# Kernel tuning notes

Measured on AMD Instinct MI355X. Metric: run time of the kernel, lower is better.

Reference implementation:

```python
import jax, jax.numpy as jnp
import numpy as np

T, H, I, E, K = 2048, 1024, 768, 32, 4  # tokens, hidden, expert intermediate, n_experts, top_k


def setup_inputs() -> dict:
    key = jax.random.key(0)
    k0, k1, k2, k3, k4 = jax.random.split(key, 5)
    scale = 0.02
    return {
        "x": jax.random.normal(k0, (T, H), dtype=jnp.float32),
        "gate_w": jax.random.normal(k1, (E, H), dtype=jnp.float32) * scale,   # router linear [E, H]
        "w_gate": jax.random.normal(k2, (E, I, H), dtype=jnp.float32) * scale,  # gate_proj per expert
        "w_up": jax.random.normal(k3, (E, I, H), dtype=jnp.float32) * scale,    # up_proj per expert
        "w_down": jax.random.normal(k4, (E, H, I), dtype=jnp.float32) * scale,  # down_proj per expert
    }


def reference(x, gate_w, w_gate, w_up, w_down):
    # Router: dense gate linear + softmax + top-k + renormalize
    logits = x @ gate_w.T                              # [T, E]
    probs = jax.nn.softmax(logits, axis=-1)
    top_w, top_i = jax.lax.top_k(probs, K)             # [T, K]
    top_w = top_w / jnp.sum(top_w, axis=-1, keepdims=True)  # renormalize=True
    # Dense combine weights [T, E] (zero for unselected experts)
    tok = jnp.arange(T, dtype=jnp.int32)[:, None]
    combine = jnp.zeros((T, E), dtype=x.dtype).at[tok, top_i].add(top_w)

    # Scan over experts: each expert is a SwiGLU MLP; masked-dense combine.
    def step(acc, ws):
        w1, w3, w2, ce = ws                            # [I,H], [I,H], [H,I], [T]
        h = (jax.nn.silu(x @ w1.T) * (x @ w3.T)) @ w2.T  # [T, H]
        return acc + ce[:, None] * h, None

    out, _ = jax.lax.scan(step, jnp.zeros_like(x), (w_gate, w_up, w_down, combine.T))
    return out
```

## Files before the change

### kernel.cpp

```cpp
#include <hip/hip_runtime.h>
#include <hip/hip_bf16.h>
#include <stdint.h>

#define T_TOK 2048
#define HDIM  1024
#define IDIM  768
#define NEXP  32
#define TOPK  4
#define NPAIR (T_TOK*TOPK)
#define MTILE 256
#define MAXMT 64

typedef __attribute__((ext_vector_type(8))) short bf16x8;
typedef __attribute__((ext_vector_type(4))) float f32x4;

__device__ __forceinline__ unsigned short f2bf(float f){
  union { float f; unsigned u; } v; v.f = f;
  unsigned r = (v.u + 0x7fffu + ((v.u >> 16) & 1u)) >> 16;
  return (unsigned short)r;
}

__global__ __launch_bounds__(256) void k_convert_x(const float* __restrict__ x,
                                                   ushort* __restrict__ xb){
  int idx = blockIdx.x*256 + threadIdx.x;
  float4 v = ((const float4*)x)[idx];
  ushort4 o; o.x=f2bf(v.x); o.y=f2bf(v.y); o.z=f2bf(v.z); o.w=f2bf(v.w);
  ((ushort4*)xb)[idx] = o;
}

__global__ __launch_bounds__(256) void k_router(const float* __restrict__ x,
                                                const float* __restrict__ gw,
                                                int* __restrict__ ei, float* __restrict__ wv,
                                                int* __restrict__ counts){
  int wid  = threadIdx.x >> 6;
  int lane = threadIdx.x & 63;
  int t = blockIdx.x*4 + wid;
  float xv[16];
  #pragma unroll
  for (int i=0;i<16;i++) xv[i] = x[t*HDIM + i*64 + lane];
  float p[NEXP];
  #pragma unroll
  for (int e=0;e<NEXP;e++){
    const float* w = gw + e*HDIM;
    float a = 0.f;
    #pragma unroll
    for (int i=0;i<16;i++) a = fmaf(xv[i], w[i*64+lane], a);
    #pragma unroll
    for (int off=32; off>=1; off>>=1) a += __shfl_xor(a, off, 64);
    p[e] = a;
  }
  float m = p[0];
  #pragma unroll
  for (int e=1;e<NEXP;e++) m = fmaxf(m, p[e]);
  #pragma unroll
  for (int e=0;e<NEXP;e++) p[e] = __expf(p[e]-m);
  unsigned used = 0; int sel[TOPK]; float sw[TOPK]; float wsum = 0.f;
  #pragma unroll
  for (int k=0;k<TOPK;k++){
    float best = -1.f; int bi = 0;
    #pragma unroll
    for (int e=0;e<NEXP;e++){
      bool ok = (((used>>e)&1u)==0u) && (p[e] > best);
      best = ok ? p[e] : best; bi = ok ? e : bi;
    }
    used |= 1u<<bi; sel[k]=bi; sw[k]=best; wsum += best;
  }
  if (lane==0){
    float inv = 1.f/wsum;
    #pragma unroll
    for (int k=0;k<TOPK;k++){
      ei[t*TOPK+k] = sel[k];
      wv[t*TOPK+k] = sw[k]*inv;
      atomicAdd(&counts[sel[k]], 1);
    }
  }
}

__global__ void k_offsets(const int* __restrict__ counts, int* __restrict__ offsets,
                          int* __restrict__ mtE, int* __restrict__ mtM0,
                          int* __restrict__ nmt){
  if (threadIdx.x==0 && blockIdx.x==0){
    int s=0;
    for (int e=0;e<NEXP;e++){ offsets[e]=s; s+=counts[e]; }
    offsets[NEXP]=s;
    int nm=0;
    for (int e=0;e<NEXP;e++){
      int ne = counts[e];
      for (int m0=0; m0<ne && nm<MAXMT; m0+=MTILE){ mtE[nm]=e; mtM0[nm]=m0; nm++; }
    }
    nmt[0]=nm;
  }
}

__global__ __launch_bounds__(256) void k_scatter(const int* __restrict__ ei,
                                                 const int* __restrict__ offsets,
                                                 int* __restrict__ cursor,
                                                 int* __restrict__ slot_tk,
                                                 int* __restrict__ tk_slot){
  int g = blockIdx.x*256 + threadIdx.x;
  int e = ei[g];
  int pos = atomicAdd(&cursor[e], 1);
  int slot = offsets[e] + pos;
  slot_tk[slot] = g;
  tk_slot[g] = slot;
}

__global__ __launch_bounds__(512,4) void k_gateup(const ushort* __restrict__ xb,
    const float* __restrict__ w1, const float* __restrict__ w3,
    const int* __restrict__ offsets, const int* __restrict__ slot_tk,
    const int* __restrict__ mtE, const int* __restrict__ mtM0, const int* __restrict__ nmt,
    ushort* __restrict__ act){
  int bi  = blockIdx.x;
  int mti = bi / 24;
  int it  = bi - mti*24;
  if (mti >= nmt[0]) return;
  int e    = mtE[mti];
  int m0   = mtM0[mti];
  int off0 = offsets[e];
  int ne   = offsets[e+1]-off0;
  int ibase = it*32;

  __shared__ int toks[256];
  __shared__ ushort Bls[2][2][32][68];

  int tid = threadIdx.x, wid = tid>>6, lane = tid&63;
  if (tid < 256){
    int slot = off0 + m0 + tid;
    int fb = slot_tk[off0] >> 2;
    toks[tid] = (m0 + tid < ne) ? (slot_tk[slot] >> 2) : fb;
  }
  int b_r = tid>>4, b_c4 = tid&15;
  const size_t wbase = (size_t)e * IDIM * HDIM;
  const float* bsrc0 = w1 + wbase + (size_t)(ibase+b_r)*HDIM + b_c4*4;
  const float* bsrc1 = w3 + wbase + (size_t)(ibase+b_r)*HDIM + b_c4*4;
  __syncthreads();

  const ushort* arow0 = xb + (size_t)toks[wid*32      + (lane&15)]*HDIM + (lane>>4)*8;
  const ushort* arow1 = xb + (size_t)toks[wid*32 + 16 + (lane&15)]*HDIM + (lane>>4)*8;

  f32x4 accg[2][2], accu[2][2];
  #pragma unroll
  for (int a=0;a<2;a++)
    #pragma unroll
    for (int b=0;b<2;b++){ accg[a][b]=(f32x4){0,0,0,0}; accu[a][b]=(f32x4){0,0,0,0}; }

  float4 bP[2], bQ[2];
  bf16x8 afA[4], afB[4];

  auto loadB = [&](int kb, float4* d){
    d[0] = *(const float4*)(bsrc0 + kb*64);
    d[1] = *(const float4*)(bsrc1 + kb*64);
  };
  auto loadA = [&](int kb, bf16x8* d){
    #pragma unroll
    for (int kk=0;kk<2;kk++){
      d[kk*2+0] = *(const bf16x8*)(arow0 + kb*64 + kk*32);
      d[kk*2+1] = *(const bf16x8*)(arow1 + kb*64 + kk*32);
    }
  };
  auto writeB = [&](int buf, const float4* s){
    #pragma unroll
    for (int m=0;m<2;m++){
      ushort4 o; o.x=f2bf(s[m].x); o.y=f2bf(s[m].y); o.z=f2bf(s[m].z); o.w=f2bf(s[m].w);
      *(ushort4*)(&Bls[buf][m][b_r][b_c4*4]) = o;
    }
  };
  auto compute = [&](int buf, const bf16x8* af){
    #pragma unroll
    for (int kk=0;kk<2;kk++){
      #pragma unroll
      for (int n=0;n<2;n++){
        bf16x8 bg = *(const bf16x8*)(&Bls[buf][0][n*16 + (lane&15)][kk*32 + (lane>>4)*8]);
        bf16x8 bu = *(const bf16x8*)(&Bls[buf][1][n*16 + (lane&15)][kk*32 + (lane>>4)*8]);
        #pragma unroll
        for (int m=0;m<2;m++){
          accg[m][n] = __builtin_amdgcn_mfma_f32_16x16x32_bf16(af[kk*2+m], bg, accg[m][n], 0,0,0);
          accu[m][n] = __builtin_amdgcn_mfma_f32_16x16x32_bf16(af[kk*2+m], bu, accu[m][n], 0,0,0);
        }
      }
    }
  };

  loadB(0, bP);
  loadA(0, afA);
  loadB(1, bQ);
  writeB(0, bP);
  __syncthreads();
  loadA(1, afB);

  for (int kb=0; kb<16; kb+=2){
    if (kb+2 < 16) loadB(kb+2, bP);
    compute(0, afA);
    if (kb+2 < 16) loadA(kb+2, afA);
    writeB(1, bQ);
    __syncthreads();
    if (kb+3 < 16) loadB(kb+3, bQ);
    compute(1, afB);
    if (kb+3 < 16) loadA(kb+3, afB);
    if (kb+2 < 16) writeB(0, bP);
    __syncthreads();
  }

  int nval = ne - m0; if (nval > 256) nval = 256;
  #pragma unroll
  for (int m=0;m<2;m++)
    #pragma unroll
    for (int n=0;n<2;n++)
      #pragma unroll
      for (int r=0;r<4;r++){
        int row = wid*32 + m*16 + (lane>>4)*4 + r;
        if (row < nval){
          float g = accg[m][n][r], u = accu[m][n][r];
          float sval = g / (1.f + __expf(-g)) * u;
          act[(size_t)(off0+m0+row)*IDIM + ibase + n*16 + (lane&15)] = f2bf(sval);
        }
      }
}

__global__ __launch_bounds__(512,4) void k_down(const ushort* __restrict__ act,
    const float* __restrict__ w2, const int* __restrict__ offsets,
    const int* __restrict__ mtE, const int* __restrict__ mtM0, const int* __restrict__ nmt,
    float* __restrict__ pout){
  int bi  = blockIdx.x;
  int mti = bi >> 4;
  int ht  = bi & 15;
  if (mti >= nmt[0]) return;
  int e    = mtE[mti];
  int m0   = mtM0[mti];
  int off0 = offsets[e], ne = offsets[e+1]-off0;
  int hbase = ht*64;

  __shared__ ushort Bls[2][64][68];

  int tid = threadIdx.x, wid = tid>>6, lane = tid&63;
  int b_r = tid>>4, b_c4 = tid&15;
  const size_t wbase = (size_t)e * HDIM * IDIM;
  const float* bsrc0 = w2 + wbase + (size_t)(hbase+b_r   )*IDIM + b_c4*4;
  const float* bsrc1 = w2 + wbase + (size_t)(hbase+b_r+32)*IDIM + b_c4*4;

  int row0 = m0 + wid*32      + (lane&15); row0 = (row0 < ne) ? row0 : 0;
  int row1 = m0 + wid*32 + 16 + (lane&15); row1 = (row1 < ne) ? row1 : 0;
  const ushort* arow0 = act + (size_t)(off0+row0)*IDIM + (lane>>4)*8;
  const ushort* arow1 = act + (size_t)(off0+row1)*IDIM + (lane>>4)*8;

  f32x4 acc[2][4];
  #pragma unroll
  for (int a=0;a<2;a++)
    #pragma unroll
    for (int b=0;b<4;b++) acc[a][b]=(f32x4){0,0,0,0};

  float4 bP[2], bQ[2];
  bf16x8 afA[4], afB[4];

  auto loadB = [&](int kb, float4* d){
    d[0] = *(const float4*)(bsrc0 + kb*64);
    d[1] = *(const float4*)(bsrc1 + kb*64);
  };
  auto loadA = [&](int kb, bf16x8* d){
    #pragma unroll
    for (int kk=0;kk<2;kk++){
      d[kk*2+0] = *(const bf16x8*)(arow0 + kb*64 + kk*32);
      d[kk*2+1] = *(const bf16x8*)(arow1 + kb*64 + kk*32);
    }
  };
  auto writeB = [&](int buf, const float4* s){
    #pragma unroll
    for (int m=0;m<2;m++){
      ushort4 o; o.x=f2bf(s[m].x); o.y=f2bf(s[m].y); o.z=f2bf(s[m].z); o.w=f2bf(s[m].w);
      *(ushort4*)(&Bls[buf][b_r + m*32][b_c4*4]) = o;
    }
  };
  auto compute = [&](int buf, const bf16x8* af){
    #pragma unroll
    for (int kk=0;kk<2;kk++){
      #pragma unroll
      for (int n=0;n<4;n++){
        bf16x8 bw = *(const bf16x8*)(&Bls[buf][n*16 + (lane&15)][kk*32 + (lane>>4)*8]);
        #pragma unroll
        for (int m=0;m<2;m++)
          acc[m][n] = __builtin_amdgcn_mfma_f32_16x16x32_bf16(af[kk*2+m], bw, acc[m][n], 0,0,0);
      }
    }
  };

  loadB(0, bP);
  loadA(0, afA);
  loadB(1, bQ);
  writeB(0, bP);
  __syncthreads();
  loadA(1, afB);

  for (int kb=0; kb<12; kb+=2){
    if (kb+2 < 12) loadB(kb+2, bP);
    compute(0, afA);
    if (kb+2 < 12) loadA(kb+2, afA);
    writeB(1, bQ);
    __syncthreads();
    if (kb+3 < 12) loadB(kb+3, bQ);
    compute(1, afB);
    if (kb+3 < 12) loadA(kb+3, afB);
    if (kb+2 < 12) writeB(0, bP);
    __syncthreads();
  }

  int nval = ne - m0; if (nval > 256) nval = 256;
  #pragma unroll
  for (int m=0;m<2;m++)
    #pragma unroll
    for (int n=0;n<4;n++)
      #pragma unroll
      for (int r=0;r<4;r++){
        int row = wid*32 + m*16 + (lane>>4)*4 + r;
        if (row < nval)
          pout[(size_t)(off0+m0+row)*HDIM + hbase + n*16 + (lane&15)] = acc[m][n][r];
      }
}

__global__ __launch_bounds__(256) void k_combine(const float* __restrict__ pout,
    const int* __restrict__ tk_slot, const float* __restrict__ wv,
    float* __restrict__ out){
  int t = blockIdx.x;
  int c = threadIdx.x;
  float a0=0,a1=0,a2=0,a3=0;
  #pragma unroll
  for (int k=0;k<TOPK;k++){
    int slot = tk_slot[t*TOPK+k];
    float w  = wv[t*TOPK+k];
    float4 v = *(const float4*)(pout + (size_t)slot*HDIM + c*4);
    a0 = fmaf(w, v.x, a0); a1 = fmaf(w, v.y, a1);
    a2 = fmaf(w, v.z, a2); a3 = fmaf(w, v.w, a3);
  }
  float4 o; o.x=a0; o.y=a1; o.z=a2; o.w=a3;
  *(float4*)(out + (size_t)t*HDIM + c*4) = o;
}

extern "C" void kernel_launch(void* const* d_in, const int* in_sizes, int n_in,
                              void* d_out, int out_size, void* d_ws, size_t ws_size,
                              hipStream_t stream){
  const float* x  = (const float*)d_in[0];
  const float* gw = (const float*)d_in[1];
  const float* w1 = (const float*)d_in[2];
  const float* w3 = (const float*)d_in[3];
  const float* w2 = (const float*)d_in[4];
  float* out = (float*)d_out;

  char* ws = (char*)d_ws;
  size_t off = 0;
  ushort* xb   = (ushort*)(ws + off); off += (size_t)T_TOK*HDIM*2;
  ushort* act  = (ushort*)(ws + off); off += (size_t)NPAIR*IDIM*2;
  float*  pout = (float*) (ws + off); off += (size_t)NPAIR*HDIM*4;
  int* counts  = (int*)(ws + off); off += NEXP*4;
  int* cursor  = (int*)(ws + off); off += NEXP*4;
  int* offsets = (int*)(ws + off); off += (NEXP+1)*4;
  int* mtE     = (int*)(ws + off); off += MAXMT*4;
  int* mtM0    = (int*)(ws + off); off += MAXMT*4;
  int* nmt     = (int*)(ws + off); off += 4;
  off = (off + 255) & ~(size_t)255;
  int*   ei      = (int*)  (ws + off); off += (size_t)NPAIR*4;
  float* wvp     = (float*)(ws + off); off += (size_t)NPAIR*4;
  int*   slot_tk = (int*)  (ws + off); off += (size_t)NPAIR*4;
  int*   tk_slot = (int*)  (ws + off); off += (size_t)NPAIR*4;

  hipMemsetAsync(counts, 0, 2*NEXP*4, stream);

  k_convert_x<<<T_TOK*HDIM/1024, 256, 0, stream>>>(x, xb);
  k_router<<<T_TOK/4, 256, 0, stream>>>(x, gw, ei, wvp, counts);
  k_offsets<<<1, 64, 0, stream>>>(counts, offsets, mtE, mtM0, nmt);
  k_scatter<<<NPAIR/256, 256, 0, stream>>>(ei, offsets, cursor, slot_tk, tk_slot);
  k_gateup<<<MAXMT*24, 512, 0, stream>>>(xb, w1, w3, offsets, slot_tk, mtE, mtM0, nmt, act);
  k_down<<<MAXMT*16, 512, 0, stream>>>(act, w2, offsets, mtE, mtM0, nmt, pout);
  k_combine<<<T_TOK, 256, 0, stream>>>(pout, tk_slot, wvp, out);
}
```

Baseline: 242.9 us.

## Stage A and B tiles via direct global-to-LDS loads with swizzled fp32 weights

Both grouped GEMM kernels now use global_load_lds to copy token activations and fp32 weight tiles straight into shared memory, double-buffered with a K-step of 32. The per-thread register staging and store-time bf16 conversion are removed. Weights are now converted to bf16 at LDS read time, using an XOR swizzle to avoid bank conflicts. The warp tiling changes to a 4x2 layout with four M sub-tiles per warp. This cuts register pressure and VALU work in the load path, but it doubles the number of barriers per K and repeats the fp32-to-bf16 conversion for each warp that reads a B tile.

```diff
diff --git a/kernel.cpp b/kernel.cpp
--- a/kernel.cpp
+++ b/kernel.cpp
@@ -13,6 +13,13 @@
 
 typedef __attribute__((ext_vector_type(8))) short bf16x8;
 typedef __attribute__((ext_vector_type(4))) float f32x4;
+
+typedef __attribute__((address_space(1))) const unsigned int gu32;
+typedef __attribute__((address_space(3))) unsigned int lu32;
+
+__device__ __forceinline__ void gload_lds16(const void* g, void* l){
+  __builtin_amdgcn_global_load_lds((gu32*)g, (lu32*)l, 16, 0, 0);
+}
 
 __device__ __forceinline__ unsigned short f2bf(float f){
   union { float f; unsigned u; } v; v.f = f;
@@ -120,8 +127,9 @@
   int ne   = offsets[e+1]-off0;
   int ibase = it*32;
 
+  __shared__ ushort Als[2][256][32];
+  __shared__ float  Bls[2][2][32][32];
   __shared__ int toks[256];
-  __shared__ ushort Bls[2][2][32][68];
 
   int tid = threadIdx.x, wid = tid>>6, lane = tid&63;
   if (tid < 256){
@@ -129,92 +137,80 @@
     int fb = slot_tk[off0] >> 2;
     toks[tid] = (m0 + tid < ne) ? (slot_tk[slot] >> 2) : fb;
   }
-  int b_r = tid>>4, b_c4 = tid&15;
-  const size_t wbase = (size_t)e * IDIM * HDIM;
-  const float* bsrc0 = w1 + wbase + (size_t)(ibase+b_r)*HDIM + b_c4*4;
-  const float* bsrc1 = w3 + wbase + (size_t)(ibase+b_r)*HDIM + b_c4*4;
   __syncthreads();
 
-  const ushort* arow0 = xb + (size_t)toks[wid*32      + (lane&15)]*HDIM + (lane>>4)*8;
-  const ushort* arow1 = xb + (size_t)toks[wid*32 + 16 + (lane&15)]*HDIM + (lane>>4)*8;
-
-  f32x4 accg[2][2], accu[2][2];
-  #pragma unroll
-  for (int a=0;a<2;a++)
-    #pragma unroll
-    for (int b=0;b<2;b++){ accg[a][b]=(f32x4){0,0,0,0}; accu[a][b]=(f32x4){0,0,0,0}; }
-
-  float4 bP[2], bQ[2];
-  bf16x8 afA[4], afB[4];
-
-  auto loadB = [&](int kb, float4* d){
-    d[0] = *(const float4*)(bsrc0 + kb*64);
-    d[1] = *(const float4*)(bsrc1 + kb*64);
+  const ushort* asrc0 = xb + (size_t)toks[      wid*16 + (lane>>2)]*HDIM + (lane&3)*8;
+  const ushort* asrc1 = xb + (size_t)toks[128 + wid*16 + (lane>>2)]*HDIM + (lane&3)*8;
+  int brow = wid*8 + (lane>>3);
+  int bmat = brow>>5, birow = brow&31, bc = lane&7;
+  const float* bsrc = (bmat ? w3 : w1) + (size_t)e*IDIM*HDIM
+                    + (size_t)(ibase+birow)*HDIM + ((bc ^ (birow&7))<<2);
+
+  int wm = wid>>1, wn = wid&1;
+  f32x4 accg[4], accu[4];
+  #pragma unroll
+  for (int m=0;m<4;m++){ accg[m]=(f32x4){0,0,0,0}; accu[m]=(f32x4){0,0,0,0}; }
+
+  ushort* aDst0 = &Als[0][0][0] + (size_t)(      wid*16)*32;
+  ushort* aDst1 = &Als[0][0][0] + (size_t)(128 + wid*16)*32;
+  float*  bDst  = &Bls[0][0][0][0] + (size_t)wid*256;
+  const size_t aBufStride = 256*32;
+  const size_t bBufStride = 2*32*32;
+
+  auto stage = [&](int buf, int kb){
+    gload_lds16(asrc0 + kb*32, aDst0 + buf*aBufStride);
+    gload_lds16(asrc1 + kb*32, aDst1 + buf*aBufStride);
+    gload_lds16(bsrc  + kb*32, bDst  + buf*bBufStride);
   };
-  auto loadA = [&](int kb, bf16x8* d){
-    #pragma unroll
-    for (int kk=0;kk<2;kk++){
-      d[kk*2+0] = *(const bf16x8*)(arow0 + kb*64 + kk*32);
-      d[kk*2+1] = *(const bf16x8*)(arow1 + kb*64 + kk*32);
+  int rB = wn*16 + (lane&15);
+  int q  = lane>>4;
+  int c1 = ( 2*q   ) ^ (rB&7);
+  int c2 = ( 2*q+1 ) ^ (rB&7);
+  auto compute = [&](int buf){
+    bf16x8 af[4];
+    #pragma unroll
+    for (int m=0;m<4;m++)
+      af[m] = *(const bf16x8*)(&Als[buf][wm*64 + m*16 + (lane&15)][q*8]);
+    #pragma unroll
+    for (int mat=0; mat<2; ++mat){
+      f32x4 x1 = *(const f32x4*)(&Bls[buf][mat][rB][c1*4]);
+      f32x4 x2 = *(const f32x4*)(&Bls[buf][mat][rB][c2*4]);
+      bf16x8 b;
+      b[0]=(short)f2bf(x1[0]); b[1]=(short)f2bf(x1[1]);
+      b[2]=(short)f2bf(x1[2]); b[3]=(short)f2bf(x1[3]);
+      b[4]=(short)f2bf(x2[0]); b[5]=(short)f2bf(x2[1]);
+      b[6]=(short)f2bf(x2[2]); b[7]=(short)f2bf(x2[3]);
+      if (mat==0){
+        #pragma unroll
+        for (int m=0;m<4;m++) accg[m] = __builtin_amdgcn_mfma_f32_16x16x32_bf16(af[m], b, accg[m], 0,0,0);
+      } else {
+        #pragma unroll
+        for (int m=0;m<4;m++) accu[m] = __builtin_amdgcn_mfma_f32_16x16x32_bf16(af[m], b, accu[m], 0,0,0);
+      }
     }
   };
-  auto writeB = [&](int buf, const float4* s){
-    #pragma unroll
-    for (int m=0;m<2;m++){
-      ushort4 o; o.x=f2bf(s[m].x); o.y=f2bf(s[m].y); o.z=f2bf(s[m].z); o.w=f2bf(s[m].w);
-      *(ushort4*)(&Bls[buf][m][b_r][b_c4*4]) = o;
-    }
-  };
-  auto compute = [&](int buf, const bf16x8* af){
-    #pragma unroll
-    for (int kk=0;kk<2;kk++){
-      #pragma unroll
-      for (int n=0;n<2;n++){
-        bf16x8 bg = *(const bf16x8*)(&Bls[buf][0][n*16 + (lane&15)][kk*32 + (lane>>4)*8]);
-        bf16x8 bu = *(const bf16x8*)(&Bls[buf][1][n*16 + (lane&15)][kk*32 + (lane>>4)*8]);
-        #pragma unroll
-        for (int m=0;m<2;m++){
-          accg[m][n] = __builtin_amdgcn_mfma_f32_16x16x32_bf16(af[kk*2+m], bg, accg[m][n], 0,0,0);
-          accu[m][n] = __builtin_amdgcn_mfma_f32_16x16x32_bf16(af[kk*2+m], bu, accu[m][n], 0,0,0);
-        }
+
+  stage(0, 0);
+  __syncthreads();
+  for (int kb=0; kb<32; ++kb){
+    int cur = kb & 1;
+    if (kb+1 < 32) stage(cur^1, kb+1);
+    compute(cur);
+    __syncthreads();
+  }
+
+  int nval = ne - m0; if (nval > 256) nval = 256;
+  #pragma unroll
+  for (int m=0;m<4;m++)
+    #pragma unroll
+    for (int r=0;r<4;r++){
+      int row = wm*64 + m*16 + (lane>>4)*4 + r;
+      if (row < nval){
+        float g = accg[m][r], u = accu[m][r];
+        float sval = g / (1.f + __expf(-g)) * u;
+        act[(size_t)(off0+m0+row)*IDIM + ibase + wn*16 + (lane&15)] = f2bf(sval);
       }
     }
-  };
-
-  loadB(0, bP);
-  loadA(0, afA);
-  loadB(1, bQ);
-  writeB(0, bP);
-  __syncthreads();
-  loadA(1, afB);
-
-  for (int kb=0; kb<16; kb+=2){
-    if (kb+2 < 16) loadB(kb+2, bP);
-    compute(0, afA);
-    if (kb+2 < 16) loadA(kb+2, afA);
-    writeB(1, bQ);
-    __syncthreads();
-    if (kb+3 < 16) loadB(kb+3, bQ);
-    compute(1, afB);
-    if (kb+3 < 16) loadA(kb+3, afB);
-    if (kb+2 < 16) writeB(0, bP);
-    __syncthreads();
-  }
-
-  int nval = ne - m0; if (nval > 256) nval = 256;
-  #pragma unroll
-  for (int m=0;m<2;m++)
-    #pragma unroll
-    for (int n=0;n<2;n++)
-      #pragma unroll
-      for (int r=0;r<4;r++){
-        int row = wid*32 + m*16 + (lane>>4)*4 + r;
-        if (row < nval){
-          float g = accg[m][n][r], u = accu[m][n][r];
-          float sval = g / (1.f + __expf(-g)) * u;
-          act[(size_t)(off0+m0+row)*IDIM + ibase + n*16 + (lane&15)] = f2bf(sval);
-        }
-      }
 }
 
 __global__ __launch_bounds__(512,4) void k_down(const ushort* __restrict__ act,
@@ -230,89 +226,81 @@
   int off0 = offsets[e], ne = offsets[e+1]-off0;
   int hbase = ht*64;
 
-  __shared__ ushort Bls[2][64][68];
+  __shared__ ushort Als[2][256][32];
+  __shared__ float  Bls[2][64][32];
 
   int tid = threadIdx.x, wid = tid>>6, lane = tid&63;
-  int b_r = tid>>4, b_c4 = tid&15;
-  const size_t wbase = (size_t)e * HDIM * IDIM;
-  const float* bsrc0 = w2 + wbase + (size_t)(hbase+b_r   )*IDIM + b_c4*4;
-  const float* bsrc1 = w2 + wbase + (size_t)(hbase+b_r+32)*IDIM + b_c4*4;
-
-  int row0 = m0 + wid*32      + (lane&15); row0 = (row0 < ne) ? row0 : 0;
-  int row1 = m0 + wid*32 + 16 + (lane&15); row1 = (row1 < ne) ? row1 : 0;
-  const ushort* arow0 = act + (size_t)(off0+row0)*IDIM + (lane>>4)*8;
-  const ushort* arow1 = act + (size_t)(off0+row1)*IDIM + (lane>>4)*8;
-
-  f32x4 acc[2][4];
-  #pragma unroll
-  for (int a=0;a<2;a++)
-    #pragma unroll
-    for (int b=0;b<4;b++) acc[a][b]=(f32x4){0,0,0,0};
-
-  float4 bP[2], bQ[2];
-  bf16x8 afA[4], afB[4];
-
-  auto loadB = [&](int kb, float4* d){
-    d[0] = *(const float4*)(bsrc0 + kb*64);
-    d[1] = *(const float4*)(bsrc1 + kb*64);
+
+  int ar0 = m0 +       wid*16 + (lane>>2); ar0 = (ar0 < ne) ? ar0 : (ne-1);
+  int ar1 = m0 + 128 + wid*16 + (lane>>2); ar1 = (ar1 < ne) ? ar1 : (ne-1);
+  const ushort* asrc0 = act + (size_t)(off0+ar0)*IDIM + (lane&3)*8;
+  const ushort* asrc1 = act + (size_t)(off0+ar1)*IDIM + (lane&3)*8;
+  int brow = wid*8 + (lane>>3);
+  int bc   = lane&7;
+  const float* bsrc = w2 + (size_t)e*HDIM*IDIM
+                    + (size_t)(hbase+brow)*IDIM + ((bc ^ (brow&7))<<2);
+
+  int wm = wid>>1, wn = wid&1;
+  f32x4 acc[4][2];
+  #pragma unroll
+  for (int m=0;m<4;m++)
+    #pragma unroll
+    for (int n=0;n<2;n++) acc[m][n]=(f32x4){0,0,0,0};
+
+  ushort* aDst0 = &Als[0][0][0] + (size_t)(      wid*16)*32;
+  ushort* aDst1 = &Als[0][0][0] + (size_t)(128 + wid*16)*32;
+  float*  bDst  = &Bls[0][0][0] + (size_t)wid*256;
+  const size_t aBufStride = 256*32;
+  const size_t bBufStride = 64*32;
+
+  auto stage = [&](int buf, int kb){
+    gload_lds16(asrc0 + kb*32, aDst0 + buf*aBufStride);
+    gload_lds16(asrc1 + kb*32, aDst1 + buf*aBufStride);
+    gload_lds16(bsrc  + kb*32, bDst  + buf*bBufStride);
   };
-  auto loadA = [&](int kb, bf16x8* d){
-    #pragma unroll
-    for (int kk=0;kk<2;kk++){
-      d[kk*2+0] = *(const bf16x8*)(arow0 + kb*64 + kk*32);
-      d[kk*2+1] = *(const bf16x8*)(arow1 + kb*64 + kk*32);
+  int q = lane>>4;
+  auto compute = [&](int buf){
+    bf16x8 af[4];
+    #pragma unroll
+    for (int m=0;m<4;m++)
+      af[m] = *(const bf16x8*)(&Als[buf][wm*64 + m*16 + (lane&15)][q*8]);
+    #pragma unroll
+    for (int n=0;n<2;n++){
+      int rB = wn*32 + n*16 + (lane&15);
+      int c1 = ( 2*q   ) ^ (rB&7);
+      int c2 = ( 2*q+1 ) ^ (rB&7);
+      f32x4 x1 = *(const f32x4*)(&Bls[buf][rB][c1*4]);
+      f32x4 x2 = *(const f32x4*)(&Bls[buf][rB][c2*4]);
+      bf16x8 b;
+      b[0]=(short)f2bf(x1[0]); b[1]=(short)f2bf(x1[1]);
+      b[2]=(short)f2bf(x1[2]); b[3]=(short)f2bf(x1[3]);
+      b[4]=(short)f2bf(x2[0]); b[5]=(short)f2bf(x2[1]);
+      b[6]=(short)f2bf(x2[2]); b[7]=(short)f2bf(x2[3]);
+      #pragma unroll
+      for (int m=0;m<4;m++)
+        acc[m][n] = __builtin_amdgcn_mfma_f32_16x16x32_bf16(af[m], b, acc[m][n], 0,0,0);
     }
   };
-  auto writeB = [&](int buf, const float4* s){
-    #pragma unroll
-    for (int m=0;m<2;m++){
-      ushort4 o; o.x=f2bf(s[m].x); o.y=f2bf(s[m].y); o.z=f2bf(s[m].z); o.w=f2bf(s[m].w);
-      *(ushort4*)(&Bls[buf][b_r + m*32][b_c4*4]) = o;
-    }
-  };
-  auto compute = [&](int buf, const bf16x8* af){
-    #pragma unroll
-    for (int kk=0;kk<2;kk++){
-      #pragma unroll
-      for (int n=0;n<4;n++){
-        bf16x8 bw = *(const bf16x8*)(&Bls[buf][n*16 + (lane&15)][kk*32 + (lane>>4)*8]);
-        #pragma unroll
-        for (int m=0;m<2;m++)
-          acc[m][n] = __builtin_amdgcn_mfma_f32_16x16x32_bf16(af[kk*2+m], bw, acc[m][n], 0,0,0);
-      }
-    }
-  };
-
-  loadB(0, bP);
-  loadA(0, afA);
-  loadB(1, bQ);
-  writeB(0, bP);
+
+  stage(0, 0);
   __syncthreads();
-  loadA(1, afB);
-
-  for (int kb=0; kb<12; kb+=2){
-    if (kb+2 < 12) loadB(kb+2, bP);
-    compute(0, afA);
-    if (kb+2 < 12) loadA(kb+2, afA);
-    writeB(1, bQ);
+  for (int kb=0; kb<24; ++kb){
+    int cur = kb & 1;
+    if (kb+1 < 24) stage(cur^1, kb+1);
+    compute(cur);
     __syncthreads();
-    if (kb+3 < 12) loadB(kb+3, bQ);
-    compute(1, afB);
-    if (kb+3 < 12) loadA(kb+3, afB);
-    if (kb+2 < 12) writeB(0, bP);
-    __syncthreads();
   }
 
   int nval = ne - m0; if (nval > 256) nval = 256;
   #pragma unroll
-  for (int m=0;m<2;m++)
-    #pragma unroll
-    for (int n=0;n<4;n++)
+  for (int m=0;m<4;m++)
+    #pragma unroll
+    for (int n=0;n<2;n++)
       #pragma unroll
       for (int r=0;r<4;r++){
-        int row = wid*32 + m*16 + (lane>>4)*4 + r;
+        int row = wm*64 + m*16 + (lane>>4)*4 + r;
         if (row < nval)
-          pout[(size_t)(off0+m0+row)*HDIM + hbase + n*16 + (lane&15)] = acc[m][n][r];
+          pout[(size_t)(off0+m0+row)*HDIM + hbase + wn*32 + n*16 + (lane&15)] = acc[m][n][r];
       }
 }
 
```

Result: slower. 270.6 us (+11.4%).
